# Optimization experiments

Hardware: AMD Instinct MI355X
Metric: run time of the kernel (lower is better)

## Reference

```python
import jax, jax.numpy as jnp
import numpy as np

B, NS, S, H = 2048, 8, 8, 512   # batch, num_units, num_mem_slots, hidden==num_mem_size
WH, WK = 1, 32                  # write attention heads, key_size
RH, RK = 4, 32                  # read (mem) attention heads, mem_attention_key


def _lin(x, W, b):
    # torch nn.Linear convention: W is [out, in]
    return jnp.einsum('...i,oi->...o', x, W) + b


def setup_inputs() -> dict:
    key = jax.random.key(0)
    ks = jax.random.split(key, 13)
    def w(k, o, i):
        return jax.random.normal(k, (o, i), jnp.float32) * 0.02
    d = {
        'h_s': jax.random.normal(ks[0], (B, NS, H), jnp.float32),
        'mem': jax.random.normal(ks[1], (B, S, H), jnp.float32),
        'wq_w': w(ks[2], WH * WK, H), 'wq_b': jnp.zeros((WH * WK,), jnp.float32),
        'wk_w': w(ks[3], WH * WK, H), 'wk_b': jnp.zeros((WH * WK,), jnp.float32),
        'wv_w': w(ks[4], WH * H, H), 'wv_b': jnp.zeros((WH * H,), jnp.float32),
        'wo_w': w(ks[5], H, WH * H), 'wo_b': jnp.zeros((H,), jnp.float32),
        'ut_w': w(ks[6], H, H),      'ut_b': jnp.zeros((H,), jnp.float32),
        'ug_w': w(ks[7], 2 * H, H),  'ug_b': jnp.zeros((2 * H,), jnp.float32),
        'rq_w': w(ks[8], RH * RK, H), 'rq_b': jnp.zeros((RH * RK,), jnp.float32),
        'rk_w': w(ks[9], RH * RK, H), 'rk_b': jnp.zeros((RH * RK,), jnp.float32),
        'rv_w': w(ks[10], RH * H, H), 'rv_b': jnp.zeros((RH * H,), jnp.float32),
        'ro_w': w(ks[11], H, RH * H), 'ro_b': jnp.zeros((H,), jnp.float32),
    }
    return d


def _forward(h_s, mem, wq_w, wq_b, wk_w, wk_b, wv_w, wv_b, wo_w, wo_b,
             ut_w, ut_b, ug_w, ug_b, rq_w, rq_b, rk_w, rk_b, rv_w, rv_b,
             ro_w, ro_b):
    b = h_s.shape[0]
    T = NS + S  # concat length for write keys/values

    # ---------------- write ----------------
    xi = jnp.concatenate([h_s, mem], axis=1)                       # [B, T, H]
    q = _lin(mem, wq_w, wq_b).reshape(b, S, WH, WK).transpose(0, 2, 1, 3)   # [B,WH,S,WK]
    k = _lin(xi, wk_w, wk_b).reshape(b, T, WH, WK).transpose(0, 2, 1, 3)    # [B,WH,T,WK]
    v = _lin(xi, wv_w, wv_b).reshape(b, T, WH, H).transpose(0, 2, 1, 3)     # [B,WH,T,H]
    scores = jnp.einsum('bhsk,bhtk->bhst', q, k) / np.sqrt(WK).astype(np.float32)
    probs = jax.nn.softmax(scores, axis=-1)                         # [B,WH,S,T]
    ctx = jnp.einsum('bhst,bhtd->bhsd', probs, v)                   # [B,WH,S,H]
    ctx = ctx.transpose(0, 2, 1, 3).reshape(b, S, WH * H)
    mem_write = _lin(ctx, wo_w, wo_b)                               # [B,S,H]

    # ---------------- update (GRU-like gating) ----------------
    inputs_mean = jax.nn.relu(_lin(h_s, ut_w, ut_b)).mean(axis=1, keepdims=True)  # [B,1,H]
    kk = inputs_mean + jnp.tanh(mem)                                # [B,S,H]
    gates = jax.nn.sigmoid(_lin(kk, ug_w, ug_b))                    # [B,S,2H]
    input_gate, forget_gate = gates[..., :H], gates[..., H:]
    mem_new = input_gate * jnp.tanh(mem_write) + forget_gate * mem  # [B,S,H]

    # ---------------- read ----------------
    q = _lin(h_s, rq_w, rq_b).reshape(b, NS, RH, RK).transpose(0, 2, 1, 3)      # [B,RH,NS,RK]
    k = _lin(mem_new, rk_w, rk_b).reshape(b, S, RH, RK).transpose(0, 2, 1, 3)   # [B,RH,S,RK]
    v = _lin(mem_new, rv_w, rv_b).reshape(b, S, RH, H).transpose(0, 2, 1, 3)    # [B,RH,S,H]
    scores = jnp.einsum('bhnk,bhsk->bhns', q, k) / np.sqrt(RK).astype(np.float32)
    probs = jax.nn.softmax(scores, axis=-1)                          # [B,RH,NS,S]
    ctx = jnp.einsum('bhns,bhsd->bhnd', probs, v)                    # [B,RH,NS,H]
    ctx = ctx.transpose(0, 2, 1, 3).reshape(b, NS, RH * H)
    h_out = h_s + _lin(ctx, ro_w, ro_b)                              # residual
    return h_out, mem_new


def reference(h_s, mem, wq_w, wq_b, wk_w, wk_b, wv_w, wv_b, wo_w, wo_b,
              ut_w, ut_b, ug_w, ug_b, rq_w, rq_b, rk_w, rk_b, rv_w, rv_b,
              ro_w, ro_b):
    return _forward(h_s, mem, wq_w, wq_b, wk_w, wk_b, wv_w, wv_b, wo_w, wo_b,
                    ut_w, ut_b, ug_w, ug_b, rq_w, rq_b, rk_w, rk_b, rv_w, rv_b,
                    ro_w, ro_b)
```

## Files before the change

### kernel.cpp

```cpp
#include <hip/hip_runtime.h>

#define Bb   2048
#define Mrows 16384
#define Hd   512

typedef float  f32x4  __attribute__((ext_vector_type(4)));
typedef __bf16 bf16x8 __attribute__((ext_vector_type(8)));
typedef unsigned short us8 __attribute__((ext_vector_type(8)));

__device__ __forceinline__ unsigned short f2bf(float f) {
    unsigned int u = __builtin_bit_cast(unsigned int, f);
    u = u + 0x7FFFu + ((u >> 16) & 1u);
    return (unsigned short)(u >> 16);
}
__device__ __forceinline__ float bf2f(unsigned short h) {
    unsigned int u = ((unsigned int)h) << 16;
    return __builtin_bit_cast(float, u);
}

#define MB (1024ull*1024ull)
#define OFF_WQ   0ull
#define OFF_WK   32768ull
#define OFF_WV   65536ull
#define OFF_WO   589824ull
#define OFF_UT   1114112ull
#define OFF_UG   1638400ull
#define OFF_RQ   2686976ull
#define OFF_RK   2818048ull
#define OFF_RV   2949120ull
#define OFF_RO   5046272ull
#define OFF_HS    (8*MB)
#define OFF_MEM   (24*MB)
#define OFF_UTR   (40*MB)
#define OFF_MEAN  (56*MB)
#define OFF_Q1    (60*MB)
#define OFF_K1    (62*MB)
#define OFF_V1    (66*MB)
#define OFF_CTX1  (100*MB)
#define OFF_KK    (116*MB)
#define OFF_TMW   (132*MB)
#define OFF_GATES (148*MB)
#define OFF_MNB   (180*MB)
#define OFF_Q2    (196*MB)
#define OFF_K2    (204*MB)
#define OFF_RVO   (40*MB)
#define OFF_CTX2  (104*MB)

struct CastSeg { const float* src; unsigned short* dst; int n4; };
struct CastParams { CastSeg seg[12]; };

__global__ __launch_bounds__(256) void cast_all(CastParams p) {
    CastSeg s = p.seg[blockIdx.y];
    int stride = gridDim.x * blockDim.x;
    for (int i = blockIdx.x * blockDim.x + threadIdx.x; i < s.n4; i += stride) {
        float4 v = reinterpret_cast<const float4*>(s.src)[i];
        ushort4 o;
        o.x = f2bf(v.x); o.y = f2bf(v.y); o.z = f2bf(v.z); o.w = f2bf(v.w);
        reinterpret_cast<ushort4*>(s.dst)[i] = o;
    }
}

template<int MODE>
__device__ __forceinline__ void store_c(void* out, const float* extra, int row,
                                        int col, int ldo, int remap_off, float v) {
    if (MODE == 0) {
        ((float*)out)[(size_t)row * ldo + col] = v;
    } else if (MODE == 1) {
        ((unsigned short*)out)[(size_t)row * ldo + col] = f2bf(v);
    } else if (MODE == 2) {
        ((unsigned short*)out)[(size_t)row * ldo + col] = f2bf(fmaxf(v, 0.f));
    } else if (MODE == 3) {
        ((unsigned short*)out)[(size_t)row * ldo + col] = f2bf(1.f / (1.f + expf(-v)));
    } else if (MODE == 4) {
        ((unsigned short*)out)[(size_t)row * ldo + col] = f2bf(tanhf(v));
    } else if (MODE == 5) {
        int rr = ((row >> 3) << 4) + (row & 7) + remap_off;
        ((float*)out)[(size_t)rr * ldo + col] = v;
    } else if (MODE == 6) {
        int rr = ((row >> 3) << 4) + (row & 7) + remap_off;
        ((unsigned short*)out)[(size_t)rr * ldo + col] = f2bf(v);
    } else if (MODE == 7) {
        ((float*)out)[(size_t)row * ldo + col] = v + extra[(size_t)row * ldo + col];
    }
}

template<int K, int MODE>
__global__ __launch_bounds__(256, 2) void gemm_big(
    const unsigned short* __restrict__ A, const unsigned short* __restrict__ W,
    const float* __restrict__ bias, void* __restrict__ out,
    const float* __restrict__ extra, int N, int ldo, int remap_off)
{
    constexpr int NT = K / 64;
    __shared__ __align__(16) unsigned short As[128 * 64];
    __shared__ __align__(16) unsigned short Bs[128 * 64];

    const int tiles_n = N >> 7;
    const int bm = (int)blockIdx.x / tiles_n;
    const int bn = (int)blockIdx.x - bm * tiles_n;
    const int t = threadIdx.x;
    const int wave = t >> 6, lane = t & 63;
    const int wr = (wave >> 1) * 64;
    const int wc = (wave & 1) * 64;
    const int lrow = lane & 15;
    const int lkh  = lane >> 4;

    const int srow = t >> 3;
    const int sch  = t & 7;
    const unsigned short* ag = A + (size_t)(bm * 128 + srow) * K + sch * 8;
    const unsigned short* bg = W + (size_t)(bn * 128 + srow) * K + sch * 8;

    int wofs[4];
    #pragma unroll
    for (int i = 0; i < 4; i++) {
        int row = srow + 32 * i;
        wofs[i] = row * 64 + ((sch ^ (row & 7)) << 3);
    }

    int aof[4][2], bof[4][2];
    #pragma unroll
    for (int m = 0; m < 4; m++) {
        int ra = wr + m * 16 + lrow;
        int rb = wc + m * 16 + lrow;
        #pragma unroll
        for (int kk = 0; kk < 2; kk++) {
            int kc = kk * 4 + lkh;
            aof[m][kk] = ra * 64 + ((kc ^ (ra & 7)) << 3);
            bof[m][kk] = rb * 64 + ((kc ^ (rb & 7)) << 3);
        }
    }

    us8 ar[4], br[4];
    f32x4 acc[4][4] = {};

    #pragma unroll
    for (int i = 0; i < 4; i++) {
        ar[i] = *reinterpret_cast<const us8*>(ag + (size_t)(32 * i) * K);
        br[i] = *reinterpret_cast<const us8*>(bg + (size_t)(32 * i) * K);
    }

    for (int kt = 0; kt < NT; ++kt) {
        #pragma unroll
        for (int i = 0; i < 4; i++) {
            *reinterpret_cast<us8*>(&As[wofs[i]]) = ar[i];
            *reinterpret_cast<us8*>(&Bs[wofs[i]]) = br[i];
        }
        __syncthreads();
        if (kt + 1 < NT) {
            const unsigned short* ag2 = ag + (kt + 1) * 64;
            const unsigned short* bg2 = bg + (kt + 1) * 64;
            #pragma unroll
            for (int i = 0; i < 4; i++) {
                ar[i] = *reinterpret_cast<const us8*>(ag2 + (size_t)(32 * i) * K);
                br[i] = *reinterpret_cast<const us8*>(bg2 + (size_t)(32 * i) * K);
            }
        }
        #pragma unroll
        for (int kk = 0; kk < 2; kk++) {
            bf16x8 af[4], bf_[4];
            #pragma unroll
            for (int m = 0; m < 4; m++)
                af[m] = __builtin_bit_cast(bf16x8,
                            *reinterpret_cast<const us8*>(&As[aof[m][kk]]));
            #pragma unroll
            for (int n = 0; n < 4; n++)
                bf_[n] = __builtin_bit_cast(bf16x8,
                            *reinterpret_cast<const us8*>(&Bs[bof[n][kk]]));
            #pragma unroll
            for (int m = 0; m < 4; m++)
                #pragma unroll
                for (int n = 0; n < 4; n++)
                    acc[m][n] = __builtin_amdgcn_mfma_f32_16x16x32_bf16(
                                    af[m], bf_[n], acc[m][n], 0, 0, 0);
        }
        __syncthreads();
    }

    #pragma unroll
    for (int n = 0; n < 4; n++) {
        int col = bn * 128 + wc + n * 16 + lrow;
        float bv = bias[col];
        #pragma unroll
        for (int m = 0; m < 4; m++) {
            #pragma unroll
            for (int r = 0; r < 4; r++) {
                int row = bm * 128 + wr + m * 16 + lkh * 4 + r;
                store_c<MODE>(out, extra, row, col, ldo, remap_off,
                              acc[m][n][r] + bv);
            }
        }
    }
}

template<int TN, int MODE, int K>
__global__ __launch_bounds__(256) void gemm_small(
    const unsigned short* __restrict__ A, const unsigned short* __restrict__ W,
    const float* __restrict__ bias, void* __restrict__ out,
    const float* __restrict__ extra, int N, int ldo, int remap_off)
{
    constexpr int BN = 16 * TN;
    const int tiles_n = N / BN;
    const int bm = blockIdx.x / tiles_n;
    const int bn = blockIdx.x % tiles_n;
    const int wave = threadIdx.x >> 6;
    const int lane = threadIdx.x & 63;
    const int row0 = bm * 64 + wave * 16;
    const int col0 = bn * BN;
    const int lrow = lane & 15;
    const int lk   = (lane >> 4) << 3;

    f32x4 acc[TN] = {};
    const unsigned short* ap  = A + (size_t)(row0 + lrow) * K + lk;
    const unsigned short* wp0 = W + (size_t)(col0 + lrow) * K + lk;

    #pragma unroll 4
    for (int ks = 0; ks < K; ks += 32) {
        bf16x8 af = __builtin_bit_cast(bf16x8,
                        *reinterpret_cast<const us8*>(ap + ks));
        #pragma unroll
        for (int tt = 0; tt < TN; tt++) {
            bf16x8 bfm = __builtin_bit_cast(bf16x8,
                        *reinterpret_cast<const us8*>(wp0 + (size_t)tt * 16 * K + ks));
            acc[tt] = __builtin_amdgcn_mfma_f32_16x16x32_bf16(af, bfm, acc[tt], 0, 0, 0);
        }
    }

    #pragma unroll
    for (int tt = 0; tt < TN; tt++) {
        int col = col0 + tt * 16 + lrow;
        float bv = bias[col];
        #pragma unroll
        for (int r = 0; r < 4; r++) {
            int row = row0 + (lane >> 4) * 4 + r;
            store_c<MODE>(out, extra, row, col, ldo, remap_off, acc[tt][r] + bv);
        }
    }
}

__global__ __launch_bounds__(256) void mean_kernel(
    const unsigned short* __restrict__ UTR, float* __restrict__ MEAN)
{
    int idx = blockIdx.x * blockDim.x + threadIdx.x;
    if (idx >= Bb * Hd) return;
    int b = idx >> 9, j = idx & 511;
    float s = 0.f;
    #pragma unroll
    for (int r = 0; r < 8; r++)
        s += bf2f(UTR[((size_t)(b * 8 + r) << 9) + j]);
    MEAN[idx] = s * 0.125f;
}

__global__ __launch_bounds__(256) void kk_kernel(
    const float* __restrict__ MEAN, const float* __restrict__ mem,
    unsigned short* __restrict__ KK)
{
    int idx = blockIdx.x * blockDim.x + threadIdx.x;
    int m = idx >> 9;
    int bj = ((m >> 3) << 9) + (idx & 511);
    KK[idx] = f2bf(MEAN[bj] + tanhf(mem[idx]));
}

__global__ __launch_bounds__(256) void memnew_kernel(
    const unsigned short* __restrict__ GATES, const unsigned short* __restrict__ TMW,
    const float* __restrict__ mem, float* __restrict__ out_mem,
    unsigned short* __restrict__ MNB)
{
    int idx = blockIdx.x * blockDim.x + threadIdx.x;
    int m = idx >> 9, j = idx & 511;
    float ig = bf2f(GATES[(size_t)m * 1024 + j]);
    float fg = bf2f(GATES[(size_t)m * 1024 + 512 + j]);
    float v  = ig * bf2f(TMW[idx]) + fg * mem[idx];
    out_mem[idx] = v;
    MNB[idx] = f2bf(v);
}

__global__ __launch_bounds__(256) void attn1_kernel(
    const float* __restrict__ Q1, const float* __restrict__ K1,
    const unsigned short* __restrict__ V1, unsigned short* __restrict__ CTX1)
{
    int b = blockIdx.x, t = threadIdx.x;
    __shared__ float q[8][32], k[16][32], pr[8][16];
    q[t >> 5][t & 31] = Q1[(size_t)b * 256 + t];
    k[t >> 5][t & 31]       = K1[(size_t)b * 512 + t];
    k[8 + (t >> 5)][t & 31] = K1[(size_t)b * 512 + 256 + t];
    __syncthreads();
    if (t < 128) {
        int s = t >> 4, tt = t & 15;
        float acc = 0.f;
        #pragma unroll
        for (int i = 0; i < 32; i++) acc += q[s][i] * k[tt][i];
        pr[s][tt] = acc * 0.17677669529663687f;
    }
    __syncthreads();
    if (t < 8) {
        float m = -1e30f;
        for (int i = 0; i < 16; i++) m = fmaxf(m, pr[t][i]);
        float e[16], sum = 0.f;
        for (int i = 0; i < 16; i++) { e[i] = expf(pr[t][i] - m); sum += e[i]; }
        float inv = 1.f / sum;
        for (int i = 0; i < 16; i++) pr[t][i] = e[i] * inv;
    }
    __syncthreads();
    int s = t >> 5, d0 = (t & 31) * 16;
    float a[16];
    #pragma unroll
    for (int i = 0; i < 16; i++) a[i] = 0.f;
    for (int tt = 0; tt < 16; tt++) {
        float p = pr[s][tt];
        const unsigned short* vp = V1 + ((size_t)(b * 16 + tt)) * 512 + d0;
        us8 v0 = *reinterpret_cast<const us8*>(vp);
        us8 v1 = *reinterpret_cast<const us8*>(vp + 8);
        #pragma unroll
        for (int i = 0; i < 8; i++) a[i]     += p * bf2f(v0[i]);
        #pragma unroll
        for (int i = 0; i < 8; i++) a[8 + i] += p * bf2f(v1[i]);
    }
    us8 o0, o1;
    #pragma unroll
    for (int i = 0; i < 8; i++) { o0[i] = f2bf(a[i]); o1[i] = f2bf(a[8 + i]); }
    unsigned short* cp = CTX1 + ((size_t)(b * 8 + s)) * 512 + d0;
    *reinterpret_cast<us8*>(cp) = o0;
    *reinterpret_cast<us8*>(cp + 8) = o1;
}

__global__ __launch_bounds__(256) void attn2_kernel(
    const float* __restrict__ Q2, const float* __restrict__ K2,
    const unsigned short* __restrict__ V2, unsigned short* __restrict__ CTX2)
{
    int b = blockIdx.x, t = threadIdx.x;
    __shared__ float q[8][128], k[8][128], pr[4][8][8];
    for (int i = t; i < 1024; i += 256) {
        q[i >> 7][i & 127] = Q2[(size_t)b * 1024 + i];
        k[i >> 7][i & 127] = K2[(size_t)b * 1024 + i];
    }
    __syncthreads();
    {
        int h = t >> 6, n = (t >> 3) & 7, s = t & 7;
        float acc = 0.f;
        #pragma unroll
        for (int i = 0; i < 32; i++) acc += q[n][h * 32 + i] * k[s][h * 32 + i];
        pr[h][n][s] = acc * 0.17677669529663687f;
    }
    __syncthreads();
    if (t < 32) {
        int h = t >> 3, n = t & 7;
        float m = -1e30f;
        for (int i = 0; i < 8; i++) m = fmaxf(m, pr[h][n][i]);
        float e[8], sum = 0.f;
        for (int i = 0; i < 8; i++) { e[i] = expf(pr[h][n][i] - m); sum += e[i]; }
        float inv = 1.f / sum;
        for (int i = 0; i < 8; i++) pr[h][n][i] = e[i] * inv;
    }
    __syncthreads();
    int n = t >> 5, d0 = (t & 31) * 16;
    for (int h = 0; h < 4; h++) {
        float a[16];
        #pragma unroll
        for (int i = 0; i < 16; i++) a[i] = 0.f;
        for (int s = 0; s < 8; s++) {
            float p = pr[h][n][s];
            const unsigned short* vp = V2 + ((size_t)(b * 8 + s)) * 2048 + h * 512 + d0;
            us8 v0 = *reinterpret_cast<const us8*>(vp);
            us8 v1 = *reinterpret_cast<const us8*>(vp + 8);
            #pragma unroll
            for (int i = 0; i < 8; i++) a[i]     += p * bf2f(v0[i]);
            #pragma unroll
            for (int i = 0; i < 8; i++) a[8 + i] += p * bf2f(v1[i]);
        }
        us8 o0, o1;
        #pragma unroll
        for (int i = 0; i < 8; i++) { o0[i] = f2bf(a[i]); o1[i] = f2bf(a[8 + i]); }
        unsigned short* cp = CTX2 + ((size_t)(b * 8 + n)) * 2048 + h * 512 + d0;
        *reinterpret_cast<us8*>(cp) = o0;
        *reinterpret_cast<us8*>(cp + 8) = o1;
    }
}

extern "C" void kernel_launch(void* const* d_in, const int* in_sizes, int n_in,
                              void* d_out, int out_size, void* d_ws, size_t ws_size,
                              hipStream_t stream)
{
    const float* h_s  = (const float*)d_in[0];
    const float* mem  = (const float*)d_in[1];
    const float* wq_w = (const float*)d_in[2];  const float* wq_b = (const float*)d_in[3];
    const float* wk_w = (const float*)d_in[4];  const float* wk_b = (const float*)d_in[5];
    const float* wv_w = (const float*)d_in[6];  const float* wv_b = (const float*)d_in[7];
    const float* wo_w = (const float*)d_in[8];  const float* wo_b = (const float*)d_in[9];
    const float* ut_w = (const float*)d_in[10]; const float* ut_b = (const float*)d_in[11];
    const float* ug_w = (const float*)d_in[12]; const float* ug_b = (const float*)d_in[13];
    const float* rq_w = (const float*)d_in[14]; const float* rq_b = (const float*)d_in[15];
    const float* rk_w = (const float*)d_in[16]; const float* rk_b = (const float*)d_in[17];
    const float* rv_w = (const float*)d_in[18]; const float* rv_b = (const float*)d_in[19];
    const float* ro_w = (const float*)d_in[20]; const float* ro_b = (const float*)d_in[21];

    char* ws = (char*)d_ws;
    unsigned short* WQb = (unsigned short*)(ws + OFF_WQ);
    unsigned short* WKb = (unsigned short*)(ws + OFF_WK);
    unsigned short* WVb = (unsigned short*)(ws + OFF_WV);
    unsigned short* WOb = (unsigned short*)(ws + OFF_WO);
    unsigned short* UTb = (unsigned short*)(ws + OFF_UT);
    unsigned short* UGb = (unsigned short*)(ws + OFF_UG);
    unsigned short* RQb = (unsigned short*)(ws + OFF_RQ);
    unsigned short* RKb = (unsigned short*)(ws + OFF_RK);
    unsigned short* RVb = (unsigned short*)(ws + OFF_RV);
    unsigned short* ROb = (unsigned short*)(ws + OFF_RO);
    unsigned short* HSb  = (unsigned short*)(ws + OFF_HS);
    unsigned short* MEMb = (unsigned short*)(ws + OFF_MEM);
    unsigned short* UTR  = (unsigned short*)(ws + OFF_UTR);
    float*          MEAN = (float*)(ws + OFF_MEAN);
    float*          Q1   = (float*)(ws + OFF_Q1);
    float*          K1   = (float*)(ws + OFF_K1);
    unsigned short* V1   = (unsigned short*)(ws + OFF_V1);
    unsigned short* CTX1 = (unsigned short*)(ws + OFF_CTX1);
    unsigned short* KKb  = (unsigned short*)(ws + OFF_KK);
    unsigned short* TMW  = (unsigned short*)(ws + OFF_TMW);
    unsigned short* GATES= (unsigned short*)(ws + OFF_GATES);
    unsigned short* MNB  = (unsigned short*)(ws + OFF_MNB);
    float*          Q2   = (float*)(ws + OFF_Q2);
    float*          K2   = (float*)(ws + OFF_K2);
    unsigned short* RVO  = (unsigned short*)(ws + OFF_RVO);
    unsigned short* CTX2 = (unsigned short*)(ws + OFF_CTX2);

    float* out   = (float*)d_out;
    float* out_m = out + (size_t)Mrows * Hd;

    CastParams cp;
    cp.seg[0]  = { h_s,  HSb,  (Mrows * Hd) / 4 };
    cp.seg[1]  = { mem,  MEMb, (Mrows * Hd) / 4 };
    cp.seg[2]  = { wq_w, WQb,  (32 * 512) / 4 };
    cp.seg[3]  = { wk_w, WKb,  (32 * 512) / 4 };
    cp.seg[4]  = { wv_w, WVb,  (512 * 512) / 4 };
    cp.seg[5]  = { wo_w, WOb,  (512 * 512) / 4 };
    cp.seg[6]  = { ut_w, UTb,  (512 * 512) / 4 };
    cp.seg[7]  = { ug_w, UGb,  (1024 * 512) / 4 };
    cp.seg[8]  = { rq_w, RQb,  (128 * 512) / 4 };
    cp.seg[9]  = { rk_w, RKb,  (128 * 512) / 4 };
    cp.seg[10] = { rv_w, RVb,  (2048 * 512) / 4 };
    cp.seg[11] = { ro_w, ROb,  (512 * 2048) / 4 };
    cast_all<<<dim3(2048, 12), 256, 0, stream>>>(cp);

    gemm_big<512,2><<<512,  256, 0, stream>>>(HSb,  UTb, ut_b, UTR, nullptr, 512, 512, 0);
    gemm_big<512,0><<<128,  256, 0, stream>>>(HSb,  RQb, rq_b, Q2,  nullptr, 128, 128, 0);
    gemm_small<2,5,512><<<256, 256, 0, stream>>>(HSb, WKb, wk_b, K1, nullptr, 32, 32, 0);
    gemm_big<512,6><<<1024, 256, 0, stream>>>(HSb,  WVb, wv_b, V1,  nullptr, 512, 512, 0);
    gemm_small<2,0,512><<<256, 256, 0, stream>>>(MEMb, WQb, wq_b, Q1, nullptr, 32, 32, 0);
    gemm_small<2,5,512><<<256, 256, 0, stream>>>(MEMb, WKb, wk_b, K1, nullptr, 32, 32, 8);
    gemm_big<512,6><<<1024, 256, 0, stream>>>(MEMb, WVb, wv_b, V1,  nullptr, 512, 512, 8);

    mean_kernel<<<4096, 256, 0, stream>>>(UTR, MEAN);
    kk_kernel<<<32768, 256, 0, stream>>>(MEAN, mem, KKb);

    attn1_kernel<<<Bb, 256, 0, stream>>>(Q1, K1, V1, CTX1);

    gemm_big<512,4><<<512,  256, 0, stream>>>(CTX1, WOb, wo_b, TMW,   nullptr,  512,  512, 0);
    gemm_big<512,3><<<1024, 256, 0, stream>>>(KKb,  UGb, ug_b, GATES, nullptr, 1024, 1024, 0);

    memnew_kernel<<<32768, 256, 0, stream>>>(GATES, TMW, mem, out_m, MNB);

    gemm_big<512,0><<<128,  256, 0, stream>>>(MNB, RKb, rk_b, K2,  nullptr,  128,  128, 0);
    gemm_big<512,1><<<2048, 256, 0, stream>>>(MNB, RVb, rv_b, RVO, nullptr, 2048, 2048, 0);

    attn2_kernel<<<Bb, 256, 0, stream>>>(Q2, K2, RVO, CTX2);

    gemm_big<2048,7><<<512, 256, 0, stream>>>(CTX2, ROb, ro_b, out, h_s, 512, 512, 0);

    (void)in_sizes; (void)n_in; (void)out_size; (void)ws_size;
}
```

Measured before the change: 554.1 us.

## Load GEMM tiles directly into LDS, swizzle block order, fix V-projection grid

The big GEMM now uses global_load_lds to copy A and W tiles straight from global memory into swizzled LDS positions, replacing the register staging step. Blocks are remapped so that consecutive blocks are spread across the grid, which is meant to improve L2 reuse. The launch-bounds occupancy hint is dropped. The two write-value projection launches are cut from 1024 to 512 blocks, removing redundant tiles that recomputed rows already covered by the other call. The tradeoff is that the next tile is now only fetched after the compute barrier, so some of the earlier load/compute overlap is lost.

After: 516.5 us. -6.8%, faster.

```diff
diff --git a/kernel.cpp b/kernel.cpp
--- a/kernel.cpp
+++ b/kernel.cpp
@@ -16,6 +16,13 @@
 __device__ __forceinline__ float bf2f(unsigned short h) {
     unsigned int u = ((unsigned int)h) << 16;
     return __builtin_bit_cast(float, u);
+}
+
+__device__ __forceinline__ void gload_lds16(const unsigned short* g, void* lds) {
+    __builtin_amdgcn_global_load_lds(
+        (const __attribute__((address_space(1))) unsigned int*)g,
+        (__attribute__((address_space(3))) unsigned int*)lds,
+        16, 0, 0);
 }
 
 #define MB (1024ull*1024ull)
@@ -85,7 +92,7 @@
 }
 
 template<int K, int MODE>
-__global__ __launch_bounds__(256, 2) void gemm_big(
+__global__ __launch_bounds__(256) void gemm_big(
     const unsigned short* __restrict__ A, const unsigned short* __restrict__ W,
     const float* __restrict__ bias, void* __restrict__ out,
     const float* __restrict__ extra, int N, int ldo, int remap_off)
@@ -94,9 +101,12 @@
     __shared__ __align__(16) unsigned short As[128 * 64];
     __shared__ __align__(16) unsigned short Bs[128 * 64];
 
+    const int nwg = (int)gridDim.x;
+    const int swz = ((int)blockIdx.x & 7) * (nwg >> 3) + ((int)blockIdx.x >> 3);
     const int tiles_n = N >> 7;
-    const int bm = (int)blockIdx.x / tiles_n;
-    const int bn = (int)blockIdx.x - bm * tiles_n;
+    const int bm = swz / tiles_n;
+    const int bn = swz - bm * tiles_n;
+
     const int t = threadIdx.x;
     const int wave = t >> 6, lane = t & 63;
     const int wr = (wave >> 1) * 64;
@@ -104,16 +114,15 @@
     const int lrow = lane & 15;
     const int lkh  = lane >> 4;
 
-    const int srow = t >> 3;
-    const int sch  = t & 7;
-    const unsigned short* ag = A + (size_t)(bm * 128 + srow) * K + sch * 8;
-    const unsigned short* bg = W + (size_t)(bn * 128 + srow) * K + sch * 8;
-
-    int wofs[4];
-    #pragma unroll
-    for (int i = 0; i < 4; i++) {
-        int row = srow + 32 * i;
-        wofs[i] = row * 64 + ((sch ^ (row & 7)) << 3);
+    const unsigned short* ga[4];
+    const unsigned short* gb[4];
+    #pragma unroll
+    for (int j = 0; j < 4; j++) {
+        int c   = wave * 256 + j * 64 + lane;
+        int row = c >> 3;
+        int kl  = (c & 7) ^ (row & 7);
+        ga[j] = A + (size_t)(bm * 128 + row) * K + kl * 8;
+        gb[j] = W + (size_t)(bn * 128 + row) * K + kl * 8;
     }
 
     int aof[4][2], bof[4][2];
@@ -129,31 +138,16 @@
         }
     }
 
-    us8 ar[4], br[4];
     f32x4 acc[4][4] = {};
 
     #pragma unroll
-    for (int i = 0; i < 4; i++) {
-        ar[i] = *reinterpret_cast<const us8*>(ag + (size_t)(32 * i) * K);
-        br[i] = *reinterpret_cast<const us8*>(bg + (size_t)(32 * i) * K);
+    for (int j = 0; j < 4; j++) {
+        gload_lds16(ga[j], (char*)As + (wave * 4 + j) * 1024);
+        gload_lds16(gb[j], (char*)Bs + (wave * 4 + j) * 1024);
     }
 
     for (int kt = 0; kt < NT; ++kt) {
-        #pragma unroll
-        for (int i = 0; i < 4; i++) {
-            *reinterpret_cast<us8*>(&As[wofs[i]]) = ar[i];
-            *reinterpret_cast<us8*>(&Bs[wofs[i]]) = br[i];
-        }
         __syncthreads();
-        if (kt + 1 < NT) {
-            const unsigned short* ag2 = ag + (kt + 1) * 64;
-            const unsigned short* bg2 = bg + (kt + 1) * 64;
-            #pragma unroll
-            for (int i = 0; i < 4; i++) {
-                ar[i] = *reinterpret_cast<const us8*>(ag2 + (size_t)(32 * i) * K);
-                br[i] = *reinterpret_cast<const us8*>(bg2 + (size_t)(32 * i) * K);
-            }
-        }
         #pragma unroll
         for (int kk = 0; kk < 2; kk++) {
             bf16x8 af[4], bf_[4];
@@ -173,6 +167,13 @@
                                     af[m], bf_[n], acc[m][n], 0, 0, 0);
         }
         __syncthreads();
+        if (kt + 1 < NT) {
+            #pragma unroll
+            for (int j = 0; j < 4; j++) {
+                gload_lds16(ga[j] + (kt + 1) * 64, (char*)As + (wave * 4 + j) * 1024);
+                gload_lds16(gb[j] + (kt + 1) * 64, (char*)Bs + (wave * 4 + j) * 1024);
+            }
+        }
     }
 
     #pragma unroll
@@ -441,10 +442,10 @@
     gemm_big<512,2><<<512,  256, 0, stream>>>(HSb,  UTb, ut_b, UTR, nullptr, 512, 512, 0);
     gemm_big<512,0><<<128,  256, 0, stream>>>(HSb,  RQb, rq_b, Q2,  nullptr, 128, 128, 0);
     gemm_small<2,5,512><<<256, 256, 0, stream>>>(HSb, WKb, wk_b, K1, nullptr, 32, 32, 0);
-    gemm_big<512,6><<<1024, 256, 0, stream>>>(HSb,  WVb, wv_b, V1,  nullptr, 512, 512, 0);
+    gemm_big<512,6><<<512,  256, 0, stream>>>(HSb,  WVb, wv_b, V1,  nullptr, 512, 512, 0);
     gemm_small<2,0,512><<<256, 256, 0, stream>>>(MEMb, WQb, wq_b, Q1, nullptr, 32, 32, 0);
     gemm_small<2,5,512><<<256, 256, 0, stream>>>(MEMb, WKb, wk_b, K1, nullptr, 32, 32, 8);
-    gemm_big<512,6><<<1024, 256, 0, stream>>>(MEMb, WVb, wv_b, V1,  nullptr, 512, 512, 8);
+    gemm_big<512,6><<<512,  256, 0, stream>>>(MEMb, WVb, wv_b, V1,  nullptr, 512, 512, 8);
 
     mean_kernel<<<4096, 256, 0, stream>>>(UTR, MEAN);
     kk_kernel<<<32768, 256, 0, stream>>>(MEAN, mem, KKb);
```
